# Performance work log

Hardware: AMD Instinct MI355X
Metric: run time of the kernel (lower is better)

## Reference

```python
import jax, jax.numpy as jnp
import numpy as np

IN_F, OUT_F = 1024, 1024
GRID_SIZE, SPLINE_ORDER = 5, 3
GRID_RANGE = (-1.0, 1.0)
NUM_BASIS = GRID_SIZE + SPLINE_ORDER  # 8


def b_splines(x, grid, spline_order):
    # x: (B, in), grid: (in, G) with G = grid_size + 2*spline_order + 1
    x = x[..., None]            # (B, in, 1)
    g = grid[None, :, :]        # (1, in, G)
    B = ((x >= g[..., :-1]) & (x < g[..., 1:])).astype(x.dtype)  # (B, in, G-1)
    for k in range(1, spline_order + 1):
        left = (x - g[..., :-(k + 1)]) / (g[..., k:-1] - g[..., :-(k + 1)])
        right = (g[..., k + 1:] - x) / (g[..., k + 1:] - g[..., 1:-k])
        B = left * B[..., :-1] + right * B[..., 1:]
    return B  # (B, in, grid_size + spline_order)


def setup_inputs() -> dict:
    key = jax.random.key(0)
    k1, k2, k3, k4 = jax.random.split(key, 4)
    batch = 8192
    x = jax.random.normal(k1, (batch, IN_F), dtype=jnp.float32)
    h = (GRID_RANGE[1] - GRID_RANGE[0]) / GRID_SIZE
    knots = jnp.arange(-SPLINE_ORDER, GRID_SIZE + SPLINE_ORDER + 1, dtype=jnp.float32) * h + GRID_RANGE[0]
    grid = jnp.broadcast_to(knots, (IN_F, knots.shape[0]))  # (in, 12)
    base_weight = jax.random.normal(k2, (OUT_F, IN_F), dtype=jnp.float32) * (1.0 / np.sqrt(IN_F))
    spline_weight = jax.random.normal(k3, (OUT_F, IN_F, NUM_BASIS), dtype=jnp.float32) * 0.02
    spline_scaler = jax.random.normal(k4, (OUT_F, IN_F), dtype=jnp.float32) * (1.0 / np.sqrt(IN_F))
    return {"x": x, "grid": grid, "base_weight": base_weight,
            "spline_weight": spline_weight, "spline_scaler": spline_scaler}


def reference(x, grid, base_weight, spline_weight, spline_scaler):
    # base branch: SiLU then linear
    base_out = jax.nn.silu(x) @ base_weight.T  # (B, out)
    # normalize x to [-1, 1] by global min/max
    x_min, x_max = jnp.min(x), jnp.max(x)
    x_norm = (x - x_min) / (x_max - x_min + 1e-8) * 2.0 - 1.0
    basis = b_splines(x_norm, grid, SPLINE_ORDER)  # (B, in, K)
    w = spline_weight * spline_scaler[..., None]   # (out, in, K)
    spline_out = jnp.einsum('bik,oik->bo', basis, w)
    return base_out + spline_out
```

## Files before the change

kernel.cpp:

```cpp
#include <hip/hip_runtime.h>
#include <hip/hip_bf16.h>

#define IN_F   1024
#define OUT_F  1024
#define NBASIS 8
#define KDIM   (IN_F + IN_F * NBASIS)
#define BK 64
#define KT      (KDIM / BK)
#define BASE_KT (IN_F / BK)

#define BM3 128
#define BN3 256
#define A_ELEMS (BM3 * BK)
#define B_ELEMS (BN3 * BK)
#define SLOT    (A_ELEMS + B_ELEMS)
#define A_OFF   0
#define B_OFF   A_ELEMS

#define BM 128
#define BN 128

typedef __attribute__((ext_vector_type(8))) short          bf16x8;
typedef __attribute__((ext_vector_type(8))) unsigned short u16x8;
typedef __attribute__((ext_vector_type(4))) float          f32x4;

typedef const __attribute__((address_space(1))) void gas_t;
typedef __attribute__((address_space(3))) void las_t;
#define GLD16(g, l) __builtin_amdgcn_global_load_lds((gas_t*)(g), (las_t*)(l), 16, 0, 0)

__device__ __forceinline__ unsigned short bfr(float f) {
    unsigned u = __float_as_uint(f);
    unsigned r = (u + 0x7FFFu + ((u >> 16) & 1u)) >> 16;
    return (unsigned short)r;
}
__device__ __forceinline__ float silu_f(float v) { return v / (1.0f + __expf(-v)); }

__device__ __forceinline__ unsigned fkey(float f) {
    unsigned u = __float_as_uint(f);
    return u ^ ((u >> 31) ? 0xFFFFFFFFu : 0x80000000u);
}
__device__ __forceinline__ float fkey_dec(unsigned u) {
    unsigned b = (u >> 31) ? (u ^ 0x80000000u) : ~u;
    return __uint_as_float(b);
}

__device__ __forceinline__ void spline8(float xv, float xmin, float scale, u16x8* o8p) {
    float xn = (xv - xmin) * scale - 1.0f;
    float u  = (xn + 2.2f) * 2.5f;
    int   iv = (int)floorf(u);
    iv = iv < 3 ? 3 : (iv > 7 ? 7 : iv);
    float tt = u - (float)iv;
    float s1 = 1.0f - tt;
    float t2 = tt * tt, t3 = t2 * tt;
    float n0 = s1 * s1 * s1 * (1.0f / 6.0f);
    float n1 = (3.0f * t3 - 6.0f * t2 + 4.0f) * (1.0f / 6.0f);
    float n2 = (-3.0f * t3 + 3.0f * t2 + 3.0f * tt + 1.0f) * (1.0f / 6.0f);
    float n3 = t3 * (1.0f / 6.0f);
    int j0 = iv - 3;
    u16x8 o8;
    #pragma unroll
    for (int s = 0; s < 8; ++s) {
        int d = s - j0;
        float val = (d == 0) ? n0 : (d == 1) ? n1 : (d == 2) ? n2 : (d == 3) ? n3 : 0.0f;
        o8[s] = bfr(val);
    }
    *o8p = o8;
}

__global__ void k_minmax(const float* __restrict__ x, unsigned* __restrict__ mm, int n4) {
    int tid    = blockIdx.x * blockDim.x + threadIdx.x;
    int stride = gridDim.x * blockDim.x;
    const float4* x4 = (const float4*)x;
    float mx  = -3.402823466e+38f;
    float mxn = -3.402823466e+38f;
    for (int i = tid; i < n4; i += stride) {
        float4 v = x4[i];
        mx  = fmaxf(mx,  fmaxf(fmaxf(v.x, v.y), fmaxf(v.z, v.w)));
        mxn = fmaxf(mxn, -fminf(fminf(v.x, v.y), fminf(v.z, v.w)));
    }
    #pragma unroll
    for (int off = 32; off; off >>= 1) {
        mx  = fmaxf(mx,  __shfl_down(mx,  off));
        mxn = fmaxf(mxn, __shfl_down(mxn, off));
    }
    __shared__ float smx[4], smn[4];
    int lane = threadIdx.x & 63, wid = threadIdx.x >> 6;
    if (lane == 0) { smx[wid] = mx; smn[wid] = mxn; }
    __syncthreads();
    if (threadIdx.x == 0) {
        #pragma unroll
        for (int w = 1; w < 4; ++w) { mx = fmaxf(mx, smx[w]); mxn = fmaxf(mxn, smn[w]); }
        atomicMax(&mm[0], fkey(mx));
        atomicMax(&mm[1], fkey(mxn));
    }
}

__global__ void k_prepw(const float* __restrict__ bw, const float* __restrict__ sw,
                        const float* __restrict__ sc, unsigned short* __restrict__ Wc) {
    int t = blockIdx.x * blockDim.x + threadIdx.x;
    int o = t >> 10, i = t & 1023;
    Wc[(size_t)o * KDIM + i] = bfr(bw[t]);
    float s = sc[t];
    const float4* swv = (const float4*)(sw + (size_t)t * 8);
    float4 a = swv[0], b = swv[1];
    u16x8 o8;
    o8[0] = bfr(a.x * s); o8[1] = bfr(a.y * s); o8[2] = bfr(a.z * s); o8[3] = bfr(a.w * s);
    o8[4] = bfr(b.x * s); o8[5] = bfr(b.y * s); o8[6] = bfr(b.z * s); o8[7] = bfr(b.w * s);
    *(u16x8*)(Wc + (size_t)o * KDIM + IN_F + i * 8) = o8;
}

__global__ void k_build_a(const float* __restrict__ x, const unsigned* __restrict__ mm,
                          unsigned short* __restrict__ Ac) {
    int t = blockIdx.x * blockDim.x + threadIdx.x;
    int row = t >> 7, i8 = t & 127;
    const float xmax  = fkey_dec(mm[0]);
    const float xmin  = -fkey_dec(mm[1]);
    const float scale = 2.0f / (xmax - xmin + 1e-8f);
    const float* xp = x + (size_t)row * IN_F + i8 * 8;
    float4 v0 = *(const float4*)xp;
    float4 v1 = *(const float4*)(xp + 4);
    size_t rb = (size_t)row * KDIM;
    u16x8 sv;
    sv[0] = bfr(silu_f(v0.x)); sv[1] = bfr(silu_f(v0.y));
    sv[2] = bfr(silu_f(v0.z)); sv[3] = bfr(silu_f(v0.w));
    sv[4] = bfr(silu_f(v1.x)); sv[5] = bfr(silu_f(v1.y));
    sv[6] = bfr(silu_f(v1.z)); sv[7] = bfr(silu_f(v1.w));
    *(u16x8*)(Ac + rb + i8 * 8) = sv;
    unsigned short* bp = Ac + rb + IN_F + (size_t)i8 * 64;
    #pragma unroll
    for (int j = 0; j < 8; ++j) {
        float xv = (j == 0) ? v0.x : (j == 1) ? v0.y : (j == 2) ? v0.z : (j == 3) ? v0.w
                 : (j == 4) ? v1.x : (j == 5) ? v1.y : (j == 6) ? v1.z : v1.w;
        u16x8 o8;
        spline8(xv, xmin, scale, &o8);
        *(u16x8*)(bp + j * 8) = o8;
    }
}

#define MFMA(a, b, c) __builtin_amdgcn_mfma_f32_16x16x32_bf16((a), (b), (c), 0, 0, 0)

__global__ __launch_bounds__(512, 2)
void k_gemm3(const unsigned short* __restrict__ Ac, const unsigned short* __restrict__ Wc,
             float* __restrict__ out) {
    __shared__ unsigned short sm[3 * SLOT];

    const int t    = threadIdx.x;
    const int lane = t & 63, w = t >> 6;
    const int bid  = blockIdx.x;
    const int xcd = bid & 7, s = bid >> 3;
    const int bM  = xcd * 8 + (s & 7);
    const int bN  = s >> 3;

    const int wave_r = w >> 2;
    const int wcq    = w & 3;

    const unsigned short* pa0; const unsigned short* pa1;
    const unsigned short* pb0; const unsigned short* pb1;
    const unsigned short* pb2; const unsigned short* pb3;
    {
        int L, r, c;
        L = (0 * 8 + w) * 64 + lane; r = L >> 3; c = L & 7;
        pa0 = Ac + (size_t)(bM * BM3 + r) * KDIM + (c ^ (r & 7)) * 8;
        L = (1 * 8 + w) * 64 + lane; r = L >> 3; c = L & 7;
        pa1 = Ac + (size_t)(bM * BM3 + r) * KDIM + (c ^ (r & 7)) * 8;
        L = (0 * 8 + w) * 64 + lane; r = L >> 3; c = L & 7;
        pb0 = Wc + (size_t)(bN * BN3 + r) * KDIM + (c ^ (r & 7)) * 8;
        L = (1 * 8 + w) * 64 + lane; r = L >> 3; c = L & 7;
        pb1 = Wc + (size_t)(bN * BN3 + r) * KDIM + (c ^ (r & 7)) * 8;
        L = (2 * 8 + w) * 64 + lane; r = L >> 3; c = L & 7;
        pb2 = Wc + (size_t)(bN * BN3 + r) * KDIM + (c ^ (r & 7)) * 8;
        L = (3 * 8 + w) * 64 + lane; r = L >> 3; c = L & 7;
        pb3 = Wc + (size_t)(bN * BN3 + r) * KDIM + (c ^ (r & 7)) * 8;
    }

    const int ach0 = (lane >> 4) ^ (lane & 7);
    const int ach1 = ach0 ^ 4;
    const int l15  = lane & 15;

    f32x4 acc[4][4] = {};

    GLD16(pa0, &sm[0 * SLOT + A_OFF + (0 * 8 + w) * 512]);
    GLD16(pa1, &sm[0 * SLOT + A_OFF + (1 * 8 + w) * 512]);
    GLD16(pb0, &sm[0 * SLOT + B_OFF + (0 * 8 + w) * 512]);
    GLD16(pb1, &sm[0 * SLOT + B_OFF + (1 * 8 + w) * 512]);
    GLD16(pb2, &sm[0 * SLOT + B_OFF + (2 * 8 + w) * 512]);
    GLD16(pb3, &sm[0 * SLOT + B_OFF + (3 * 8 + w) * 512]);
    pa0 += BK; pa1 += BK; pb0 += BK; pb1 += BK; pb2 += BK; pb3 += BK;
    GLD16(pa0, &sm[1 * SLOT + A_OFF + (0 * 8 + w) * 512]);
    GLD16(pa1, &sm[1 * SLOT + A_OFF + (1 * 8 + w) * 512]);
    GLD16(pb0, &sm[1 * SLOT + B_OFF + (0 * 8 + w) * 512]);
    GLD16(pb1, &sm[1 * SLOT + B_OFF + (1 * 8 + w) * 512]);
    GLD16(pb2, &sm[1 * SLOT + B_OFF + (2 * 8 + w) * 512]);
    GLD16(pb3, &sm[1 * SLOT + B_OFF + (3 * 8 + w) * 512]);
    pa0 += BK; pa1 += BK; pb0 += BK; pb1 += BK; pb2 += BK; pb3 += BK;

    int o0 = 0, o1 = SLOT, o2 = 2 * SLOT;
    int sk = 2;

    asm volatile("s_waitcnt vmcnt(6)" ::: "memory");
    asm volatile("s_barrier" ::: "memory");

    for (int kt = 0; kt < KT; ++kt) {
        bf16x8 af[4][2];
        #pragma unroll
        for (int mi = 0; mi < 4; ++mi) {
            int r = wave_r * 64 + mi * 16 + l15;
            af[mi][0] = *(const bf16x8*)&sm[o0 + A_OFF + r * BK + ach0 * 8];
            af[mi][1] = *(const bf16x8*)&sm[o0 + A_OFF + r * BK + ach1 * 8];
        }
        bf16x8 bf0[2][2];
        #pragma unroll
        for (int ni = 0; ni < 2; ++ni) {
            int r = wcq * 64 + ni * 16 + l15;
            bf0[ni][0] = *(const bf16x8*)&sm[o0 + B_OFF + r * BK + ach0 * 8];
            bf0[ni][1] = *(const bf16x8*)&sm[o0 + B_OFF + r * BK + ach1 * 8];
        }
        GLD16(pa0, &sm[o2 + A_OFF + (0 * 8 + w) * 512]);
        GLD16(pa1, &sm[o2 + A_OFF + (1 * 8 + w) * 512]);
        __builtin_amdgcn_s_barrier();
        __builtin_amdgcn_s_setprio(1);
        #pragma unroll
        for (int ni = 0; ni < 2; ++ni)
            #pragma unroll
            for (int mi = 0; mi < 4; ++mi) {
                acc[mi][ni] = MFMA(af[mi][0], bf0[ni][0], acc[mi][ni]);
                acc[mi][ni] = MFMA(af[mi][1], bf0[ni][1], acc[mi][ni]);
            }
        __builtin_amdgcn_s_setprio(0);
        __builtin_amdgcn_s_barrier();

        bf16x8 bf1[2][2];
        #pragma unroll
        for (int ni = 0; ni < 2; ++ni) {
            int r = wcq * 64 + (ni + 2) * 16 + l15;
            bf1[ni][0] = *(const bf16x8*)&sm[o0 + B_OFF + r * BK + ach0 * 8];
            bf1[ni][1] = *(const bf16x8*)&sm[o0 + B_OFF + r * BK + ach1 * 8];
        }
        GLD16(pb0, &sm[o2 + B_OFF + (0 * 8 + w) * 512]);
        GLD16(pb1, &sm[o2 + B_OFF + (1 * 8 + w) * 512]);
        GLD16(pb2, &sm[o2 + B_OFF + (2 * 8 + w) * 512]);
        GLD16(pb3, &sm[o2 + B_OFF + (3 * 8 + w) * 512]);
        __builtin_amdgcn_s_barrier();
        __builtin_amdgcn_s_setprio(1);
        #pragma unroll
        for (int ni = 0; ni < 2; ++ni)
            #pragma unroll
            for (int mi = 0; mi < 4; ++mi) {
                acc[mi][ni + 2] = MFMA(af[mi][0], bf1[ni][0], acc[mi][ni + 2]);
                acc[mi][ni + 2] = MFMA(af[mi][1], bf1[ni][1], acc[mi][ni + 2]);
            }
        __builtin_amdgcn_s_setprio(0);

        pa0 += BK; pa1 += BK; pb0 += BK; pb1 += BK; pb2 += BK; pb3 += BK;
        if (++sk == KT) {
            sk = 0;
            pa0 -= KDIM; pa1 -= KDIM; pb0 -= KDIM; pb1 -= KDIM; pb2 -= KDIM; pb3 -= KDIM;
        }

        asm volatile("s_waitcnt vmcnt(6)" ::: "memory");
        asm volatile("s_barrier" ::: "memory");
        int tmp = o0; o0 = o1; o1 = o2; o2 = tmp;
    }

    #pragma unroll
    for (int mi = 0; mi < 4; ++mi) {
        #pragma unroll
        for (int ni = 0; ni < 4; ++ni) {
            #pragma unroll
            for (int reg = 0; reg < 4; ++reg) {
                int row = bM * BM3 + wave_r * 64 + mi * 16 + (lane >> 4) * 4 + reg;
                int col = bN * BN3 + wcq * 64 + ni * 16 + l15;
                out[(size_t)row * OUT_F + col] = acc[mi][ni][reg];
            }
        }
    }
}

__global__ __launch_bounds__(256, 2)
void k_gemm2(const unsigned short* __restrict__ Ac, const unsigned short* __restrict__ Wc,
             float* __restrict__ out, int nmb) {
    __shared__ unsigned short As[BM * BK];
    __shared__ unsigned short Bs[BN * BK];

    const int t = threadIdx.x;
    const int lane = t & 63, w = t >> 6;
    int bid = blockIdx.x;
    int bM = bid >> 3, bN = bid & 7;

    const unsigned short* pa[4];
    const unsigned short* pb[4];
    #pragma unroll
    for (int q = 0; q < 4; ++q) {
        int idx = (q * 4 + w) * 64 + lane;
        int r = idx >> 3, c8 = idx & 7;
        pa[q] = Ac + (size_t)(bM * BM + r) * KDIM + c8 * 8;
        pb[q] = Wc + (size_t)(bN * BN + r) * KDIM + c8 * 8;
    }

    const int wr  = (w >> 1) * 64;
    const int wc2 = (w & 1) * 64;

    f32x4 acc[4][4] = {};

    for (int kt = 0; kt < KT; ++kt) {
        __syncthreads();
        #pragma unroll
        for (int q = 0; q < 4; ++q) {
            GLD16(pa[q], &As[(q * 4 + w) * 512]);
            GLD16(pb[q], &Bs[(q * 4 + w) * 512]);
            pa[q] += BK;
            pb[q] += BK;
        }
        __syncthreads();

        bf16x8 af[4][2];
        #pragma unroll
        for (int mi = 0; mi < 4; ++mi) {
            int row = wr + mi * 16 + (lane & 15);
            #pragma unroll
            for (int ks = 0; ks < 2; ++ks)
                af[mi][ks] = *(const bf16x8*)&As[row * BK + ks * 32 + (lane >> 4) * 8];
        }
        #pragma unroll
        for (int ni = 0; ni < 4; ++ni) {
            int col = wc2 + ni * 16 + (lane & 15);
            bf16x8 b0 = *(const bf16x8*)&Bs[col * BK + (lane >> 4) * 8];
            bf16x8 b1 = *(const bf16x8*)&Bs[col * BK + 32 + (lane >> 4) * 8];
            #pragma unroll
            for (int mi = 0; mi < 4; ++mi) {
                acc[mi][ni] = MFMA(af[mi][0], b0, acc[mi][ni]);
                acc[mi][ni] = MFMA(af[mi][1], b1, acc[mi][ni]);
            }
        }
    }

    #pragma unroll
    for (int mi = 0; mi < 4; ++mi) {
        #pragma unroll
        for (int ni = 0; ni < 4; ++ni) {
            #pragma unroll
            for (int reg = 0; reg < 4; ++reg) {
                int row = wr + mi * 16 + (lane >> 4) * 4 + reg;
                int col = wc2 + ni * 16 + (lane & 15);
                out[(size_t)(bM * BM + row) * OUT_F + bN * BN + col] = acc[mi][ni][reg];
            }
        }
    }
}

extern "C" void kernel_launch(void* const* d_in, const int* in_sizes, int n_in,
                              void* d_out, int out_size, void* d_ws, size_t ws_size,
                              hipStream_t stream) {
    const float* x  = (const float*)d_in[0];
    const float* bw = (const float*)d_in[2];
    const float* sw = (const float*)d_in[3];
    const float* sc = (const float*)d_in[4];
    float* out = (float*)d_out;

    const int batch = in_sizes[0] / IN_F;
    const int n4    = in_sizes[0] / 4;

    unsigned*       mm = (unsigned*)d_ws;
    unsigned short* Wc = (unsigned short*)((char*)d_ws + 512);
    const size_t    wc_bytes = (size_t)OUT_F * KDIM * 2;
    unsigned short* Ac = (unsigned short*)((char*)d_ws + 512 + wc_bytes);
    const size_t    ac_bytes = (size_t)batch * KDIM * 2;
    const size_t    need = 512 + wc_bytes + ac_bytes;

    hipMemsetAsync(d_ws, 0, 8, stream);
    k_minmax<<<1024, 256, 0, stream>>>(x, mm, n4);
    k_prepw<<<(OUT_F * IN_F) / 256, 256, 0, stream>>>(bw, sw, sc, Wc);

    if (ws_size >= need && batch == 8192) {
        k_build_a<<<(batch * 128) / 256, 256, 0, stream>>>(x, mm, Ac);
        k_gemm3<<<dim3((batch / BM3) * (OUT_F / BN3)), 512, 0, stream>>>(Ac, Wc, out);
    } else if (ws_size >= need && (batch % BM) == 0) {
        k_build_a<<<(batch * 128) / 256, 256, 0, stream>>>(x, mm, Ac);
        k_gemm2<<<dim3((batch / BM) * (OUT_F / BN)), 256, 0, stream>>>(Ac, Wc, out, batch / BM);
    }
}
```

Before: 336.3 us.

## Switch GEMM to 32x32x16 MFMA tiles and merge prep kernels into one launch

The main GEMM moves from 16x16x32 MFMA fragments to 32x32x16 bf16 MFMA with 2x2 f32x16 accumulators per wave. The LDS fragment reads change so each half of the K=64 tile is processed in two k-substeps, while the swizzled layout is kept. This cuts the number of LDS fragment reads and MFMA instructions per tile. Separately, the A-matrix build and the weight prep are fused into a single kernel launch, with one thread per x element instead of one per 8 elements, which may change memory coalescing of the spline writes. The prep kernel also now runs unconditionally, even when the workspace is too small.

New measurement: 319.9 us. 1.05x faster.

```diff
diff --git a/kernel.cpp b/kernel.cpp
--- a/kernel.cpp
+++ b/kernel.cpp
@@ -7,7 +7,6 @@
 #define KDIM   (IN_F + IN_F * NBASIS)
 #define BK 64
 #define KT      (KDIM / BK)
-#define BASE_KT (IN_F / BK)
 
 #define BM3 128
 #define BN3 256
@@ -20,9 +19,10 @@
 #define BM 128
 #define BN 128
 
-typedef __attribute__((ext_vector_type(8))) short          bf16x8;
-typedef __attribute__((ext_vector_type(8))) unsigned short u16x8;
-typedef __attribute__((ext_vector_type(4))) float          f32x4;
+typedef __attribute__((ext_vector_type(8)))  short          bf16x8;
+typedef __attribute__((ext_vector_type(8)))  unsigned short u16x8;
+typedef __attribute__((ext_vector_type(4)))  float          f32x4;
+typedef __attribute__((ext_vector_type(16))) float          f32x16;
 
 typedef const __attribute__((address_space(1))) void gas_t;
 typedef __attribute__((address_space(3))) void las_t;
@@ -95,52 +95,43 @@
     }
 }
 
-__global__ void k_prepw(const float* __restrict__ bw, const float* __restrict__ sw,
-                        const float* __restrict__ sc, unsigned short* __restrict__ Wc) {
-    int t = blockIdx.x * blockDim.x + threadIdx.x;
-    int o = t >> 10, i = t & 1023;
-    Wc[(size_t)o * KDIM + i] = bfr(bw[t]);
-    float s = sc[t];
-    const float4* swv = (const float4*)(sw + (size_t)t * 8);
-    float4 a = swv[0], b = swv[1];
-    u16x8 o8;
-    o8[0] = bfr(a.x * s); o8[1] = bfr(a.y * s); o8[2] = bfr(a.z * s); o8[3] = bfr(a.w * s);
-    o8[4] = bfr(b.x * s); o8[5] = bfr(b.y * s); o8[6] = bfr(b.z * s); o8[7] = bfr(b.w * s);
-    *(u16x8*)(Wc + (size_t)o * KDIM + IN_F + i * 8) = o8;
-}
-
-__global__ void k_build_a(const float* __restrict__ x, const unsigned* __restrict__ mm,
-                          unsigned short* __restrict__ Ac) {
-    int t = blockIdx.x * blockDim.x + threadIdx.x;
-    int row = t >> 7, i8 = t & 127;
-    const float xmax  = fkey_dec(mm[0]);
-    const float xmin  = -fkey_dec(mm[1]);
-    const float scale = 2.0f / (xmax - xmin + 1e-8f);
-    const float* xp = x + (size_t)row * IN_F + i8 * 8;
-    float4 v0 = *(const float4*)xp;
-    float4 v1 = *(const float4*)(xp + 4);
-    size_t rb = (size_t)row * KDIM;
-    u16x8 sv;
-    sv[0] = bfr(silu_f(v0.x)); sv[1] = bfr(silu_f(v0.y));
-    sv[2] = bfr(silu_f(v0.z)); sv[3] = bfr(silu_f(v0.w));
-    sv[4] = bfr(silu_f(v1.x)); sv[5] = bfr(silu_f(v1.y));
-    sv[6] = bfr(silu_f(v1.z)); sv[7] = bfr(silu_f(v1.w));
-    *(u16x8*)(Ac + rb + i8 * 8) = sv;
-    unsigned short* bp = Ac + rb + IN_F + (size_t)i8 * 64;
-    #pragma unroll
-    for (int j = 0; j < 8; ++j) {
-        float xv = (j == 0) ? v0.x : (j == 1) ? v0.y : (j == 2) ? v0.z : (j == 3) ? v0.w
-                 : (j == 4) ? v1.x : (j == 5) ? v1.y : (j == 6) ? v1.z : v1.w;
+__global__ void k_prep_all(const float* __restrict__ x, const unsigned* __restrict__ mm,
+                           const float* __restrict__ bw, const float* __restrict__ sw,
+                           const float* __restrict__ sc,
+                           unsigned short* __restrict__ Ac, unsigned short* __restrict__ Wc,
+                           int nba) {
+    int bid = blockIdx.x;
+    if (bid < nba) {
+        int t = bid * 256 + threadIdx.x;
+        int row = t >> 10, i = t & 1023;
+        const float xmax  = fkey_dec(mm[0]);
+        const float xmin  = -fkey_dec(mm[1]);
+        const float scale = 2.0f / (xmax - xmin + 1e-8f);
+        float xv = x[t];
+        size_t rb = (size_t)row * KDIM;
+        Ac[rb + i] = bfr(silu_f(xv));
         u16x8 o8;
         spline8(xv, xmin, scale, &o8);
-        *(u16x8*)(bp + j * 8) = o8;
-    }
-}
-
-#define MFMA(a, b, c) __builtin_amdgcn_mfma_f32_16x16x32_bf16((a), (b), (c), 0, 0, 0)
+        *(u16x8*)(Ac + rb + IN_F + (size_t)i * 8) = o8;
+    } else {
+        int t = (bid - nba) * 256 + threadIdx.x;
+        int o = t >> 10, i = t & 1023;
+        Wc[(size_t)o * KDIM + i] = bfr(bw[t]);
+        float s = sc[t];
+        const float4* swv = (const float4*)(sw + (size_t)t * 8);
+        float4 a = swv[0], b = swv[1];
+        u16x8 o8;
+        o8[0] = bfr(a.x * s); o8[1] = bfr(a.y * s); o8[2] = bfr(a.z * s); o8[3] = bfr(a.w * s);
+        o8[4] = bfr(b.x * s); o8[5] = bfr(b.y * s); o8[6] = bfr(b.z * s); o8[7] = bfr(b.w * s);
+        *(u16x8*)(Wc + (size_t)o * KDIM + IN_F + i * 8) = o8;
+    }
+}
+
+#define MFMA32(a, b, c) __builtin_amdgcn_mfma_f32_32x32x16_bf16((a), (b), (c), 0, 0, 0)
+#define MFMA16(a, b, c) __builtin_amdgcn_mfma_f32_16x16x32_bf16((a), (b), (c), 0, 0, 0)
 
 __global__ __launch_bounds__(512, 2)
-void k_gemm3(const unsigned short* __restrict__ Ac, const unsigned short* __restrict__ Wc,
+void k_gemm4(const unsigned short* __restrict__ Ac, const unsigned short* __restrict__ Wc,
              float* __restrict__ out) {
     __shared__ unsigned short sm[3 * SLOT];
 
@@ -153,6 +144,8 @@
 
     const int wave_r = w >> 2;
     const int wcq    = w & 3;
+    const int l31 = lane & 31;
+    const int hl  = lane >> 5;
 
     const unsigned short* pa0; const unsigned short* pa1;
     const unsigned short* pb0; const unsigned short* pb1;
@@ -173,11 +166,13 @@
         pb3 = Wc + (size_t)(bN * BN3 + r) * KDIM + (c ^ (r & 7)) * 8;
     }
 
-    const int ach0 = (lane >> 4) ^ (lane & 7);
-    const int ach1 = ach0 ^ 4;
-    const int l15  = lane & 15;
-
-    f32x4 acc[4][4] = {};
+    int rA[2], rB[2];
+    #pragma unroll
+    for (int mi = 0; mi < 2; ++mi) rA[mi] = wave_r * 64 + mi * 32 + l31;
+    #pragma unroll
+    for (int ni = 0; ni < 2; ++ni) rB[ni] = wcq * 64 + ni * 32 + l31;
+
+    f32x16 acc[2][2] = {};
 
     GLD16(pa0, &sm[0 * SLOT + A_OFF + (0 * 8 + w) * 512]);
     GLD16(pa1, &sm[0 * SLOT + A_OFF + (1 * 8 + w) * 512]);
@@ -201,55 +196,63 @@
     asm volatile("s_barrier" ::: "memory");
 
     for (int kt = 0; kt < KT; ++kt) {
-        bf16x8 af[4][2];
-        #pragma unroll
-        for (int mi = 0; mi < 4; ++mi) {
-            int r = wave_r * 64 + mi * 16 + l15;
-            af[mi][0] = *(const bf16x8*)&sm[o0 + A_OFF + r * BK + ach0 * 8];
-            af[mi][1] = *(const bf16x8*)&sm[o0 + A_OFF + r * BK + ach1 * 8];
-        }
-        bf16x8 bf0[2][2];
-        #pragma unroll
-        for (int ni = 0; ni < 2; ++ni) {
-            int r = wcq * 64 + ni * 16 + l15;
-            bf0[ni][0] = *(const bf16x8*)&sm[o0 + B_OFF + r * BK + ach0 * 8];
-            bf0[ni][1] = *(const bf16x8*)&sm[o0 + B_OFF + r * BK + ach1 * 8];
-        }
-        GLD16(pa0, &sm[o2 + A_OFF + (0 * 8 + w) * 512]);
-        GLD16(pa1, &sm[o2 + A_OFF + (1 * 8 + w) * 512]);
-        __builtin_amdgcn_s_barrier();
-        __builtin_amdgcn_s_setprio(1);
-        #pragma unroll
-        for (int ni = 0; ni < 2; ++ni)
-            #pragma unroll
-            for (int mi = 0; mi < 4; ++mi) {
-                acc[mi][ni] = MFMA(af[mi][0], bf0[ni][0], acc[mi][ni]);
-                acc[mi][ni] = MFMA(af[mi][1], bf0[ni][1], acc[mi][ni]);
-            }
-        __builtin_amdgcn_s_setprio(0);
-        __builtin_amdgcn_s_barrier();
-
-        bf16x8 bf1[2][2];
-        #pragma unroll
-        for (int ni = 0; ni < 2; ++ni) {
-            int r = wcq * 64 + (ni + 2) * 16 + l15;
-            bf1[ni][0] = *(const bf16x8*)&sm[o0 + B_OFF + r * BK + ach0 * 8];
-            bf1[ni][1] = *(const bf16x8*)&sm[o0 + B_OFF + r * BK + ach1 * 8];
-        }
-        GLD16(pb0, &sm[o2 + B_OFF + (0 * 8 + w) * 512]);
-        GLD16(pb1, &sm[o2 + B_OFF + (1 * 8 + w) * 512]);
-        GLD16(pb2, &sm[o2 + B_OFF + (2 * 8 + w) * 512]);
-        GLD16(pb3, &sm[o2 + B_OFF + (3 * 8 + w) * 512]);
-        __builtin_amdgcn_s_barrier();
-        __builtin_amdgcn_s_setprio(1);
-        #pragma unroll
-        for (int ni = 0; ni < 2; ++ni)
-            #pragma unroll
-            for (int mi = 0; mi < 4; ++mi) {
-                acc[mi][ni + 2] = MFMA(af[mi][0], bf1[ni][0], acc[mi][ni + 2]);
-                acc[mi][ni + 2] = MFMA(af[mi][1], bf1[ni][1], acc[mi][ni + 2]);
-            }
-        __builtin_amdgcn_s_setprio(0);
+        {
+            bf16x8 a0[2], a1[2], b0[2], b1[2];
+            #pragma unroll
+            for (int mi = 0; mi < 2; ++mi) {
+                int sa = rA[mi] & 7;
+                a0[mi] = *(const bf16x8*)&sm[o0 + A_OFF + rA[mi] * BK + (((0 + hl) ^ sa) << 3)];
+                a1[mi] = *(const bf16x8*)&sm[o0 + A_OFF + rA[mi] * BK + (((2 + hl) ^ sa) << 3)];
+            }
+            #pragma unroll
+            for (int ni = 0; ni < 2; ++ni) {
+                int sb = rB[ni] & 7;
+                b0[ni] = *(const bf16x8*)&sm[o0 + B_OFF + rB[ni] * BK + (((0 + hl) ^ sb) << 3)];
+                b1[ni] = *(const bf16x8*)&sm[o0 + B_OFF + rB[ni] * BK + (((2 + hl) ^ sb) << 3)];
+            }
+            GLD16(pa0, &sm[o2 + A_OFF + (0 * 8 + w) * 512]);
+            GLD16(pa1, &sm[o2 + A_OFF + (1 * 8 + w) * 512]);
+            __builtin_amdgcn_s_barrier();
+            __builtin_amdgcn_s_setprio(1);
+            #pragma unroll
+            for (int mi = 0; mi < 2; ++mi)
+                #pragma unroll
+                for (int ni = 0; ni < 2; ++ni) {
+                    acc[mi][ni] = MFMA32(a0[mi], b0[ni], acc[mi][ni]);
+                    acc[mi][ni] = MFMA32(a1[mi], b1[ni], acc[mi][ni]);
+                }
+            __builtin_amdgcn_s_setprio(0);
+            __builtin_amdgcn_s_barrier();
+        }
+        {
+            bf16x8 a0[2], a1[2], b0[2], b1[2];
+            #pragma unroll
+            for (int mi = 0; mi < 2; ++mi) {
+                int sa = rA[mi] & 7;
+                a0[mi] = *(const bf16x8*)&sm[o0 + A_OFF + rA[mi] * BK + (((4 + hl) ^ sa) << 3)];
+                a1[mi] = *(const bf16x8*)&sm[o0 + A_OFF + rA[mi] * BK + (((6 + hl) ^ sa) << 3)];
+            }
+            #pragma unroll
+            for (int ni = 0; ni < 2; ++ni) {
+                int sb = rB[ni] & 7;
+                b0[ni] = *(const bf16x8*)&sm[o0 + B_OFF + rB[ni] * BK + (((4 + hl) ^ sb) << 3)];
+                b1[ni] = *(const bf16x8*)&sm[o0 + B_OFF + rB[ni] * BK + (((6 + hl) ^ sb) << 3)];
+            }
+            GLD16(pb0, &sm[o2 + B_OFF + (0 * 8 + w) * 512]);
+            GLD16(pb1, &sm[o2 + B_OFF + (1 * 8 + w) * 512]);
+            GLD16(pb2, &sm[o2 + B_OFF + (2 * 8 + w) * 512]);
+            GLD16(pb3, &sm[o2 + B_OFF + (3 * 8 + w) * 512]);
+            __builtin_amdgcn_s_barrier();
+            __builtin_amdgcn_s_setprio(1);
+            #pragma unroll
+            for (int mi = 0; mi < 2; ++mi)
+                #pragma unroll
+                for (int ni = 0; ni < 2; ++ni) {
+                    acc[mi][ni] = MFMA32(a0[mi], b0[ni], acc[mi][ni]);
+                    acc[mi][ni] = MFMA32(a1[mi], b1[ni], acc[mi][ni]);
+                }
+            __builtin_amdgcn_s_setprio(0);
+        }
 
         pa0 += BK; pa1 += BK; pb0 += BK; pb1 += BK; pb2 += BK; pb3 += BK;
         if (++sk == KT) {
@@ -263,13 +266,13 @@
     }
 
     #pragma unroll
-    for (int mi = 0; mi < 4; ++mi) {
-        #pragma unroll
-        for (int ni = 0; ni < 4; ++ni) {
-            #pragma unroll
-            for (int reg = 0; reg < 4; ++reg) {
-                int row = bM * BM3 + wave_r * 64 + mi * 16 + (lane >> 4) * 4 + reg;
-                int col = bN * BN3 + wcq * 64 + ni * 16 + l15;
+    for (int mi = 0; mi < 2; ++mi) {
+        #pragma unroll
+        for (int ni = 0; ni < 2; ++ni) {
+            #pragma unroll
+            for (int reg = 0; reg < 16; ++reg) {
+                int row = bM * BM3 + wave_r * 64 + mi * 32 + (reg & 3) + 8 * (reg >> 2) + 4 * hl;
+                int col = bN * BN3 + wcq * 64 + ni * 32 + l31;
                 out[(size_t)row * OUT_F + col] = acc[mi][ni][reg];
             }
         }
@@ -328,8 +331,8 @@
             bf16x8 b1 = *(const bf16x8*)&Bs[col * BK + 32 + (lane >> 4) * 8];
             #pragma unroll
             for (int mi = 0; mi < 4; ++mi) {
-                acc[mi][ni] = MFMA(af[mi][0], b0, acc[mi][ni]);
-                acc[mi][ni] = MFMA(af[mi][1], b1, acc[mi][ni]);
+                acc[mi][ni] = MFMA16(af[mi][0], b0, acc[mi][ni]);
+                acc[mi][ni] = MFMA16(af[mi][1], b1, acc[mi][ni]);
             }
         }
     }
@@ -369,13 +372,13 @@
 
     hipMemsetAsync(d_ws, 0, 8, stream);
     k_minmax<<<1024, 256, 0, stream>>>(x, mm, n4);
-    k_prepw<<<(OUT_F * IN_F) / 256, 256, 0, stream>>>(bw, sw, sc, Wc);
+
+    const int nba = (batch * IN_F) / 256;
+    k_prep_all<<<nba + (OUT_F * IN_F) / 256, 256, 0, stream>>>(x, mm, bw, sw, sc, Ac, Wc, nba);
 
     if (ws_size >= need && batch == 8192) {
-        k_build_a<<<(batch * 128) / 256, 256, 0, stream>>>(x, mm, Ac);
-        k_gemm3<<<dim3((batch / BM3) * (OUT_F / BN3)), 512, 0, stream>>>(Ac, Wc, out);
+        k_gemm4<<<dim3((batch / BM3) * (OUT_F / BN3)), 512, 0, stream>>>(Ac, Wc, out);
     } else if (ws_size >= need && (batch % BM) == 0) {
-        k_build_a<<<(batch * 128) / 256, 256, 0, stream>>>(x, mm, Ac);
         k_gemm2<<<dim3((batch / BM) * (OUT_F / BN)), 256, 0, stream>>>(Ac, Wc, out, batch / BM);
     }
 }
```
